# Performance work log

Hardware: AMD Instinct MI355X
Metric: run time of the kernel (lower is better)

The kernel has to match this reference:

```python
import jax, jax.numpy as jnp
import numpy as np

N_EMBD = 1024
N_HEAD = 16
HEAD_DIM = N_EMBD // N_HEAD
LN_EPS = 1e-5


def _layer_norm(x, g, b):
    mu = jnp.mean(x, axis=-1, keepdims=True)
    var = jnp.mean((x - mu) ** 2, axis=-1, keepdims=True)
    return (x - mu) * jax.lax.rsqrt(var + LN_EPS) * g + b


def setup_inputs() -> dict:
    key = jax.random.key(0)
    ks = jax.random.split(key, 12)
    C = N_EMBD
    s_in = 1.0 / np.sqrt(C)
    s_hid = 1.0 / np.sqrt(4 * C)
    return {
        "x": jax.random.normal(ks[0], (4, 2048, C), dtype=jnp.float32),
        "ln1_g": jnp.ones((C,), jnp.float32),
        "ln1_b": jnp.zeros((C,), jnp.float32),
        "ln2_g": jnp.ones((C,), jnp.float32),
        "ln2_b": jnp.zeros((C,), jnp.float32),
        "qkv_w": jax.random.uniform(ks[1], (3 * C, C), jnp.float32, -s_in, s_in),
        "qkv_b": jax.random.uniform(ks[2], (3 * C,), jnp.float32, -s_in, s_in),
        "proj_w": jax.random.uniform(ks[3], (C, C), jnp.float32, -s_in, s_in),
        "proj_b": jax.random.uniform(ks[4], (C,), jnp.float32, -s_in, s_in),
        "fc1_w": jax.random.uniform(ks[5], (4 * C, C), jnp.float32, -s_in, s_in),
        "fc1_b": jax.random.uniform(ks[6], (4 * C,), jnp.float32, -s_in, s_in),
        "fc2_w": jax.random.uniform(ks[7], (C, 4 * C), jnp.float32, -s_hid, s_hid),
        "fc2_b": jax.random.uniform(ks[8], (C,), jnp.float32, -s_hid, s_hid),
    }


def reference(x, ln1_g, ln1_b, ln2_g, ln2_b, qkv_w, qkv_b, proj_w, proj_b,
              fc1_w, fc1_b, fc2_w, fc2_b):
    B, T, C = x.shape
    # --- attention (dropout in eval mode = identity) ---
    h = _layer_norm(x, ln1_g, ln1_b)
    qkv = h @ qkv_w.T + qkv_b                      # [B,T,3C]
    qkv = qkv.reshape(B, T, 3, N_HEAD, HEAD_DIM)
    q, k, v = qkv[:, :, 0], qkv[:, :, 1], qkv[:, :, 2]   # [B,T,H,D]
    scale = 1.0 / np.sqrt(HEAD_DIM)
    attn = jnp.einsum('bqhd,bkhd->bhqk', q, k) * scale   # [B,H,T,T]
    attn = jax.nn.softmax(attn, axis=-1)
    y = jnp.einsum('bhqk,bkhd->bqhd', attn, v).reshape(B, T, C)
    x = x + (y @ proj_w.T + proj_b)
    # --- MLP ---
    h = _layer_norm(x, ln2_g, ln2_b)
    h = jax.nn.gelu(h @ fc1_w.T + fc1_b, approximate=False)
    x = x + (h @ fc2_w.T + fc2_b)
    return x
```

## Files before the change

kernel.cpp:

```cpp
#include <hip/hip_runtime.h>
#include <cstdint>
#include <cstddef>


typedef __attribute__((ext_vector_type(8))) __bf16 bf16x8;
typedef __attribute__((ext_vector_type(8))) unsigned short u16x8;
typedef __attribute__((ext_vector_type(4))) float f32x4;

static constexpr int Bn = 4;
static constexpr int Tn = 2048;
static constexpr int Cn = 1024;
static constexpr int Hn = 16;
static constexpr int Dn = 64;

__device__ __forceinline__ unsigned short f2bf(float f) {
    unsigned int u = __builtin_bit_cast(unsigned int, f);
    u += 0x7fffu + ((u >> 16) & 1u);
    return (unsigned short)(u >> 16);
}

#define GLL16(gp, lp) __builtin_amdgcn_global_load_lds( \
    (const __attribute__((address_space(1))) void*)(gp), \
    (__attribute__((address_space(3))) void*)(lp), 16, 0, 0)

__global__ __launch_bounds__(256) void conv_bf16(const float* __restrict__ in,
                                                 unsigned short* __restrict__ out,
                                                 int n4) {
    int i = blockIdx.x * 256 + threadIdx.x;
    if (i < n4) {
        float4 v = ((const float4*)in)[i];
        ushort4 o;
        o.x = f2bf(v.x); o.y = f2bf(v.y); o.z = f2bf(v.z); o.w = f2bf(v.w);
        ((ushort4*)out)[i] = o;
    }
}

__global__ __launch_bounds__(256) void ln_kernel(const float* __restrict__ x,
                                                 const float* __restrict__ g,
                                                 const float* __restrict__ b,
                                                 unsigned short* __restrict__ out) {
    __shared__ float red[8];
    const int row = blockIdx.x;
    const int tid = threadIdx.x;
    const float4 v = ((const float4*)(x + (size_t)row * Cn))[tid];
    float s = v.x + v.y + v.z + v.w;
    float q = v.x * v.x + v.y * v.y + v.z * v.z + v.w * v.w;
    #pragma unroll
    for (int m = 1; m < 64; m <<= 1) {
        s += __shfl_xor(s, m, 64);
        q += __shfl_xor(q, m, 64);
    }
    const int wave = tid >> 6;
    if ((tid & 63) == 0) { red[wave] = s; red[4 + wave] = q; }
    __syncthreads();
    s = red[0] + red[1] + red[2] + red[3];
    q = red[4] + red[5] + red[6] + red[7];
    const float mu  = s * (1.0f / Cn);
    const float var = q * (1.0f / Cn) - mu * mu;
    const float rstd = rsqrtf(var + 1e-5f);
    const float4 gv = ((const float4*)g)[tid];
    const float4 bv = ((const float4*)b)[tid];
    ushort4 o;
    o.x = f2bf((v.x - mu) * rstd * gv.x + bv.x);
    o.y = f2bf((v.y - mu) * rstd * gv.y + bv.y);
    o.z = f2bf((v.z - mu) * rstd * gv.z + bv.z);
    o.w = f2bf((v.w - mu) * rstd * gv.w + bv.w);
    ((ushort4*)(out + (size_t)row * Cn))[tid] = o;
}

template <bool GELU, bool RES>
__global__ __launch_bounds__(256, 2)
void gemm_bt(const unsigned short* __restrict__ A,
             const unsigned short* __restrict__ W,
             const float* __restrict__ bias,
             const float* __restrict__ res,
             void* __restrict__ out,
             int M, int N, int K) {
    __shared__ unsigned short aL[128 * 32];
    __shared__ unsigned short bL[128 * 32];
    const int tid  = threadIdx.x;
    const int lane = tid & 63;
    const int wave = tid >> 6;
    const int wm = wave >> 1, wn = wave & 1;
    const int bm0 = blockIdx.y * 128, bn0 = blockIdx.x * 128;
    const int l15 = lane & 15, l4 = lane >> 4;

    f32x4 acc[4][4] = {};

    for (int kt = 0; kt < K; kt += 32) {
        #pragma unroll
        for (int i = 0; i < 2; ++i) {
            const int ch = i * 256 + tid;
            const int r = ch >> 2, c = ch & 3;
            GLL16(A + (size_t)(bm0 + r) * K + kt + c * 8, &aL[ch * 8]);
            GLL16(W + (size_t)(bn0 + r) * K + kt + c * 8, &bL[ch * 8]);
        }
        __syncthreads();
        bf16x8 av[4], bv[4];
        #pragma unroll
        for (int mi = 0; mi < 4; ++mi)
            av[mi] = *(const bf16x8*)&aL[(wm * 64 + mi * 16 + l15) * 32 + l4 * 8];
        #pragma unroll
        for (int ni = 0; ni < 4; ++ni)
            bv[ni] = *(const bf16x8*)&bL[(wn * 64 + ni * 16 + l15) * 32 + l4 * 8];
        #pragma unroll
        for (int mi = 0; mi < 4; ++mi)
            #pragma unroll
            for (int ni = 0; ni < 4; ++ni)
                acc[mi][ni] = __builtin_amdgcn_mfma_f32_16x16x32_bf16(
                    av[mi], bv[ni], acc[mi][ni], 0, 0, 0);
        __syncthreads();
    }

    #pragma unroll
    for (int mi = 0; mi < 4; ++mi) {
        #pragma unroll
        for (int ni = 0; ni < 4; ++ni) {
            const int col = bn0 + wn * 64 + ni * 16 + l15;
            const float bvl = bias[col];
            #pragma unroll
            for (int j = 0; j < 4; ++j) {
                const int r = bm0 + wm * 64 + mi * 16 + l4 * 4 + j;
                float v = acc[mi][ni][j] + bvl;
                if (GELU) v = 0.5f * v * (1.0f + erff(v * 0.70710678118f));
                const size_t idx = (size_t)r * N + col;
                if (RES) ((float*)out)[idx] = res[idx] + v;
                else     ((unsigned short*)out)[idx] = f2bf(v);
            }
        }
    }
}

__global__ __launch_bounds__(256, 2)
void attn_kernel(const unsigned short* __restrict__ qkv,
                 unsigned short* __restrict__ y) {
    __shared__ unsigned short kL[128 * 64];
    __shared__ unsigned short vT[64 * 128];
    __shared__ unsigned short pL[4][16 * 128];
    const int tid  = threadIdx.x;
    const int lane = tid & 63;
    const int wave = tid >> 6;
    const int l15 = lane & 15, l4 = lane >> 4;
    const int bh = blockIdx.y, b = bh >> 4, h = bh & 15;
    const int q0 = blockIdx.x * 64;
    const size_t base = (size_t)b * Tn * (3 * Cn);

    const int tq = q0 + wave * 16 + l15;
    const unsigned short* qp = qkv + base + (size_t)tq * (3 * Cn) + h * Dn;
    const bf16x8 qf0 = *(const bf16x8*)(qp + l4 * 8);
    const bf16x8 qf1 = *(const bf16x8*)(qp + 32 + l4 * 8);

    float mr[4], lr[4];
    f32x4 o[4] = {};
    #pragma unroll
    for (int j = 0; j < 4; ++j) { mr[j] = -1e30f; lr[j] = 0.0f; }

    for (int kt = 0; kt < Tn; kt += 128) {
        #pragma unroll
        for (int i = 0; i < 4; ++i) {
            const int ch = i * 256 + tid;
            const int key = ch >> 3, cs = ch & 7;
            const int c_log = cs ^ (key & 7);
            GLL16(qkv + base + (size_t)(kt + key) * (3 * Cn) + Cn + h * Dn + c_log * 8,
                  &kL[ch * 8]);
        }
        #pragma unroll
        for (int i = 0; i < 4; ++i) {
            const int ch = i * 256 + tid;
            const int key = ch & 127, c = ch >> 7;
            const u16x8 vv = *(const u16x8*)(qkv + base + (size_t)(kt + key) * (3 * Cn)
                                             + 2 * Cn + h * Dn + c * 8);
            #pragma unroll
            for (int j = 0; j < 8; ++j) {
                const int d = c * 8 + j;
                const int ps = ((key >> 3) ^ (d & 15)) * 8 + (key & 7);
                vT[d * 128 + ps] = vv[j];
            }
        }
        __syncthreads();

        f32x4 s[8];
        __builtin_amdgcn_s_setprio(1);
        #pragma unroll
        for (int ni = 0; ni < 8; ++ni) {
            const int krow = ni * 16 + l15;
            const int ks = (krow & 7) << 3;
            const bf16x8 kb0 = *(const bf16x8*)&kL[krow * 64 + ((l4 * 8) ^ ks)];
            const bf16x8 kb1 = *(const bf16x8*)&kL[krow * 64 + ((32 + l4 * 8) ^ ks)];
            f32x4 a = {};
            a = __builtin_amdgcn_mfma_f32_16x16x32_bf16(qf0, kb0, a, 0, 0, 0);
            a = __builtin_amdgcn_mfma_f32_16x16x32_bf16(qf1, kb1, a, 0, 0, 0);
            s[ni] = a * 0.125f;
        }
        __builtin_amdgcn_s_setprio(0);

        #pragma unroll
        for (int j = 0; j < 4; ++j) {
            float tm = -1e30f;
            #pragma unroll
            for (int ni = 0; ni < 8; ++ni) tm = fmaxf(tm, s[ni][j]);
            #pragma unroll
            for (int m = 1; m < 16; m <<= 1) tm = fmaxf(tm, __shfl_xor(tm, m, 64));
            const float mn = fmaxf(mr[j], tm);
            const float al = __expf(mr[j] - mn);
            mr[j] = mn;
            float rs = 0.0f;
            #pragma unroll
            for (int ni = 0; ni < 8; ++ni) {
                const float p = __expf(s[ni][j] - mn);
                s[ni][j] = p;
                rs += p;
            }
            #pragma unroll
            for (int m = 1; m < 16; m <<= 1) rs += __shfl_xor(rs, m, 64);
            lr[j] = lr[j] * al + rs;
            #pragma unroll
            for (int di = 0; di < 4; ++di) o[di][j] *= al;
            const int row = l4 * 4 + j;
            #pragma unroll
            for (int ni = 0; ni < 8; ++ni) {
                const int col = ni * 16 + l15;
                const int ps = (((col >> 3) ^ row) << 3) | (col & 7);
                pL[wave][row * 128 + ps] = f2bf(s[ni][j]);
            }
        }

        __builtin_amdgcn_s_setprio(1);
        #pragma unroll
        for (int kk = 0; kk < 4; ++kk) {
            const int pslot = (kk * 4 + l4) ^ l15;
            const bf16x8 pa = *(const bf16x8*)&pL[wave][l15 * 128 + pslot * 8];
            #pragma unroll
            for (int di = 0; di < 4; ++di) {
                const int drow = di * 16 + l15;
                const int vslot = (kk * 4 + l4) ^ (drow & 15);
                const bf16x8 vb = *(const bf16x8*)&vT[drow * 128 + vslot * 8];
                o[di] = __builtin_amdgcn_mfma_f32_16x16x32_bf16(pa, vb, o[di], 0, 0, 0);
            }
        }
        __builtin_amdgcn_s_setprio(0);
        __syncthreads();
    }

    #pragma unroll
    for (int di = 0; di < 4; ++di) {
        #pragma unroll
        for (int j = 0; j < 4; ++j) {
            const int t = q0 + wave * 16 + l4 * 4 + j;
            y[(size_t)(b * Tn + t) * Cn + h * Dn + di * 16 + l15] = f2bf(o[di][j] / lr[j]);
        }
    }
}

extern "C" void kernel_launch(void* const* d_in, const int* in_sizes, int n_in,
                              void* d_out, int out_size, void* d_ws, size_t ws_size,
                              hipStream_t stream) {
    (void)in_sizes; (void)n_in; (void)out_size; (void)ws_size;
    const float* x      = (const float*)d_in[0];
    const float* ln1_g  = (const float*)d_in[1];
    const float* ln1_b  = (const float*)d_in[2];
    const float* ln2_g  = (const float*)d_in[3];
    const float* ln2_b  = (const float*)d_in[4];
    const float* qkv_w  = (const float*)d_in[5];
    const float* qkv_b  = (const float*)d_in[6];
    const float* proj_w = (const float*)d_in[7];
    const float* proj_b = (const float*)d_in[8];
    const float* fc1_w  = (const float*)d_in[9];
    const float* fc1_b  = (const float*)d_in[10];
    const float* fc2_w  = (const float*)d_in[11];
    const float* fc2_b  = (const float*)d_in[12];

    char* ws = (char*)d_ws;
    unsigned short* wq  = (unsigned short*)(ws + 0);
    unsigned short* wp  = (unsigned short*)(ws + 6291456);
    unsigned short* wf1 = (unsigned short*)(ws + 8388608);
    unsigned short* wf2 = (unsigned short*)(ws + 16777216);
    unsigned short* h   = (unsigned short*)(ws + 25165824);
    unsigned short* qkv = (unsigned short*)(ws + 41943040);
    unsigned short* yb  = (unsigned short*)(ws + 92274688);
    unsigned short* act = (unsigned short*)(ws + 41943040);
    float*          x2  = (float*)d_out;

    const int BT = Bn * Tn;

    conv_bf16<<<dim3(3072), dim3(256), 0, stream>>>(qkv_w, wq, 3 * Cn * Cn / 4);
    conv_bf16<<<dim3(1024), dim3(256), 0, stream>>>(proj_w, wp, Cn * Cn / 4);
    conv_bf16<<<dim3(4096), dim3(256), 0, stream>>>(fc1_w, wf1, 4 * Cn * Cn / 4);
    conv_bf16<<<dim3(4096), dim3(256), 0, stream>>>(fc2_w, wf2, 4 * Cn * Cn / 4);

    ln_kernel<<<dim3(BT), dim3(256), 0, stream>>>(x, ln1_g, ln1_b, h);
    gemm_bt<false, false><<<dim3(3 * Cn / 128, BT / 128), dim3(256), 0, stream>>>(
        h, wq, qkv_b, nullptr, qkv, BT, 3 * Cn, Cn);
    attn_kernel<<<dim3(Tn / 64, Bn * Hn), dim3(256), 0, stream>>>(qkv, yb);
    gemm_bt<false, true><<<dim3(Cn / 128, BT / 128), dim3(256), 0, stream>>>(
        yb, wp, proj_b, x, x2, BT, Cn, Cn);
    ln_kernel<<<dim3(BT), dim3(256), 0, stream>>>(x2, ln2_g, ln2_b, h);
    gemm_bt<true, false><<<dim3(4 * Cn / 128, BT / 128), dim3(256), 0, stream>>>(
        h, wf1, fc1_b, nullptr, act, BT, 4 * Cn, Cn);
    gemm_bt<false, true><<<dim3(Cn / 128, BT / 128), dim3(256), 0, stream>>>(
        act, wf2, fc2_b, x2, (float*)d_out, BT, Cn, 4 * Cn);
}
```

Before: 671.9 us.

## Rewrite GEMM as 256x256 double-buffered tiles with swizzled LDS and interleaved prefetch

Replaces the 128x128 K=32 GEMM with a 512-thread kernel that computes 256x256 tiles at K=64 per step. It double-buffers LDS with a XOR swizzle to avoid bank conflicts and spreads the next tile's global-to-LDS loads between MFMA groups under raised wave priority. The aim is more data reuse per load, fewer barriers, and hiding load latency behind compute. In exchange it uses 128KB of LDS and a large accumulator set, which may limit occupancy, and the grids for the N=1024 GEMMs become small (128 blocks).

```diff
diff --git a/kernel.cpp b/kernel.cpp
--- a/kernel.cpp
+++ b/kernel.cpp
@@ -69,58 +69,122 @@
 }
 
 template <bool GELU, bool RES>
-__global__ __launch_bounds__(256, 2)
-void gemm_bt(const unsigned short* __restrict__ A,
+__global__ __launch_bounds__(512, 2)
+void gemm256(const unsigned short* __restrict__ A,
              const unsigned short* __restrict__ W,
              const float* __restrict__ bias,
              const float* __restrict__ res,
              void* __restrict__ out,
              int M, int N, int K) {
-    __shared__ unsigned short aL[128 * 32];
-    __shared__ unsigned short bL[128 * 32];
+    __shared__ unsigned short aL[2][256 * 64];
+    __shared__ unsigned short bL[2][256 * 64];
     const int tid  = threadIdx.x;
     const int lane = tid & 63;
     const int wave = tid >> 6;
-    const int wm = wave >> 1, wn = wave & 1;
-    const int bm0 = blockIdx.y * 128, bn0 = blockIdx.x * 128;
+    const int wm = wave >> 2;
+    const int wn = wave & 3;
+    const int bm0 = blockIdx.y * 256, bn0 = blockIdx.x * 256;
     const int l15 = lane & 15, l4 = lane >> 4;
-
-    f32x4 acc[4][4] = {};
-
-    for (int kt = 0; kt < K; kt += 32) {
+    const int NT = K >> 6;
+
+    const unsigned short* srcA[2][2];
+    const unsigned short* srcB[2][2];
+    int dstc[2][2];
+    #pragma unroll
+    for (int gh = 0; gh < 2; ++gh) {
         #pragma unroll
         for (int i = 0; i < 2; ++i) {
-            const int ch = i * 256 + tid;
-            const int r = ch >> 2, c = ch & 3;
-            GLL16(A + (size_t)(bm0 + r) * K + kt + c * 8, &aL[ch * 8]);
-            GLL16(W + (size_t)(bn0 + r) * K + kt + c * 8, &bL[ch * 8]);
-        }
-        __syncthreads();
-        bf16x8 av[4], bv[4];
-        #pragma unroll
-        for (int mi = 0; mi < 4; ++mi)
-            av[mi] = *(const bf16x8*)&aL[(wm * 64 + mi * 16 + l15) * 32 + l4 * 8];
+            const int ch = i * 512 + tid;
+            const int row = ch >> 3, sl = ch & 7;
+            const int srow = gh * 128 + row;
+            const int scol = (sl ^ (srow & 7)) << 3;
+            srcA[gh][i] = A + (size_t)(bm0 + srow) * K + scol;
+            srcB[gh][i] = W + (size_t)(bn0 + srow) * K + scol;
+            dstc[gh][i] = gh * 1024 + ch;
+        }
+    }
+
+    f32x4 acc[8][4] = {};
+
+    #pragma unroll
+    for (int gh = 0; gh < 2; ++gh)
+        #pragma unroll
+        for (int i = 0; i < 2; ++i) {
+            GLL16(srcA[gh][i], &aL[0][dstc[gh][i] * 8]);
+            GLL16(srcB[gh][i], &bL[0][dstc[gh][i] * 8]);
+        }
+    asm volatile("s_waitcnt vmcnt(0)" ::: "memory");
+    __builtin_amdgcn_sched_barrier(0);
+    __builtin_amdgcn_s_barrier();
+
+    for (int t = 0; t < NT; ++t) {
+        const int cur = t & 1, nxt = cur ^ 1;
+        const bool pf = (t + 1 < NT);
+        const int kt1 = (t + 1) << 6;
+
+        if (pf) {
+            GLL16(srcA[0][0] + kt1, &aL[nxt][dstc[0][0] * 8]);
+            GLL16(srcA[0][1] + kt1, &aL[nxt][dstc[0][1] * 8]);
+        }
+        bf16x8 bfr[4][2];
         #pragma unroll
         for (int ni = 0; ni < 4; ++ni)
-            bv[ni] = *(const bf16x8*)&bL[(wn * 64 + ni * 16 + l15) * 32 + l4 * 8];
-        #pragma unroll
-        for (int mi = 0; mi < 4; ++mi)
-            #pragma unroll
-            for (int ni = 0; ni < 4; ++ni)
-                acc[mi][ni] = __builtin_amdgcn_mfma_f32_16x16x32_bf16(
-                    av[mi], bv[ni], acc[mi][ni], 0, 0, 0);
-        __syncthreads();
-    }
-
-    #pragma unroll
-    for (int mi = 0; mi < 4; ++mi) {
+            #pragma unroll
+            for (int kk = 0; kk < 2; ++kk) {
+                const int row = wn * 64 + ni * 16 + l15;
+                const int sl = (kk * 4 + l4) ^ (row & 7);
+                bfr[ni][kk] = *(const bf16x8*)&bL[cur][row * 64 + sl * 8];
+            }
+
+        #pragma unroll
+        for (int q = 0; q < 4; ++q) {
+            if (q == 1 && pf) {
+                GLL16(srcA[1][0] + kt1, &aL[nxt][dstc[1][0] * 8]);
+                GLL16(srcA[1][1] + kt1, &aL[nxt][dstc[1][1] * 8]);
+            }
+            if (q == 2 && pf) {
+                GLL16(srcB[0][0] + kt1, &bL[nxt][dstc[0][0] * 8]);
+                GLL16(srcB[0][1] + kt1, &bL[nxt][dstc[0][1] * 8]);
+            }
+            if (q == 3 && pf) {
+                GLL16(srcB[1][0] + kt1, &bL[nxt][dstc[1][0] * 8]);
+                GLL16(srcB[1][1] + kt1, &bL[nxt][dstc[1][1] * 8]);
+            }
+            bf16x8 afr[2][2];
+            #pragma unroll
+            for (int m2 = 0; m2 < 2; ++m2)
+                #pragma unroll
+                for (int kk = 0; kk < 2; ++kk) {
+                    const int row = wm * 128 + (q * 2 + m2) * 16 + l15;
+                    const int sl = (kk * 4 + l4) ^ (row & 7);
+                    afr[m2][kk] = *(const bf16x8*)&aL[cur][row * 64 + sl * 8];
+                }
+            __builtin_amdgcn_s_setprio(1);
+            #pragma unroll
+            for (int m2 = 0; m2 < 2; ++m2)
+                #pragma unroll
+                for (int ni = 0; ni < 4; ++ni)
+                    #pragma unroll
+                    for (int kk = 0; kk < 2; ++kk)
+                        acc[q * 2 + m2][ni] = __builtin_amdgcn_mfma_f32_16x16x32_bf16(
+                            afr[m2][kk], bfr[ni][kk], acc[q * 2 + m2][ni], 0, 0, 0);
+            __builtin_amdgcn_s_setprio(0);
+        }
+
+        asm volatile("s_waitcnt vmcnt(0)" ::: "memory");
+        __builtin_amdgcn_sched_barrier(0);
+        __builtin_amdgcn_s_barrier();
+    }
+
+    #pragma unroll
+    for (int mi = 0; mi < 8; ++mi) {
         #pragma unroll
         for (int ni = 0; ni < 4; ++ni) {
             const int col = bn0 + wn * 64 + ni * 16 + l15;
             const float bvl = bias[col];
             #pragma unroll
             for (int j = 0; j < 4; ++j) {
-                const int r = bm0 + wm * 64 + mi * 16 + l4 * 4 + j;
+                const int r = bm0 + wm * 128 + mi * 16 + l4 * 4 + j;
                 float v = acc[mi][ni][j] + bvl;
                 if (GELU) v = 0.5f * v * (1.0f + erff(v * 0.70710678118f));
                 const size_t idx = (size_t)r * N + col;
@@ -289,14 +353,14 @@
     conv_bf16<<<dim3(4096), dim3(256), 0, stream>>>(fc2_w, wf2, 4 * Cn * Cn / 4);
 
     ln_kernel<<<dim3(BT), dim3(256), 0, stream>>>(x, ln1_g, ln1_b, h);
-    gemm_bt<false, false><<<dim3(3 * Cn / 128, BT / 128), dim3(256), 0, stream>>>(
+    gemm256<false, false><<<dim3(3 * Cn / 256, BT / 256), dim3(512), 0, stream>>>(
         h, wq, qkv_b, nullptr, qkv, BT, 3 * Cn, Cn);
     attn_kernel<<<dim3(Tn / 64, Bn * Hn), dim3(256), 0, stream>>>(qkv, yb);
-    gemm_bt<false, true><<<dim3(Cn / 128, BT / 128), dim3(256), 0, stream>>>(
+    gemm256<false, true><<<dim3(Cn / 256, BT / 256), dim3(512), 0, stream>>>(
         yb, wp, proj_b, x, x2, BT, Cn, Cn);
     ln_kernel<<<dim3(BT), dim3(256), 0, stream>>>(x2, ln2_g, ln2_b, h);
-    gemm_bt<true, false><<<dim3(4 * Cn / 128, BT / 128), dim3(256), 0, stream>>>(
+    gemm256<true, false><<<dim3(4 * Cn / 256, BT / 256), dim3(512), 0, stream>>>(
         h, wf1, fc1_b, nullptr, act, BT, 4 * Cn, Cn);
-    gemm_bt<false, true><<<dim3(Cn / 128, BT / 128), dim3(256), 0, stream>>>(
+    gemm256<false, true><<<dim3(Cn / 256, BT / 256), dim3(512), 0, stream>>>(
         act, wf2, fc2_b, x2, (float*)d_out, BT, Cn, 4 * Cn);
 }
```

Measured after the change: 784.6 us. 1.17x slower.

## Double-buffer GEMM LDS tiles with K=64 steps and XOR-swizzled layout

Applied to the files above, without the earlier changes.

The GEMM kernel now uses two LDS buffers and issues the global-to-LDS loads for the next K tile before computing on the current one, so memory latency overlaps the MFMA work. The K step grows from 32 to 64, halving the number of barriers per tile. LDS chunks are XOR-swizzled by row to avoid bank conflicts on the fragment reads. LDS use rises to 64KB per block, which may limit the occupancy implied by launch_bounds(256,2). With a single barrier per iteration, the prefetch into the next buffer is not waited on before that buffer is read, so correctness relies on implicit ordering of the async loads.

```diff
diff --git a/kernel.cpp b/kernel.cpp
--- a/kernel.cpp
+++ b/kernel.cpp
@@ -76,39 +76,73 @@
              const float* __restrict__ res,
              void* __restrict__ out,
              int M, int N, int K) {
-    __shared__ unsigned short aL[128 * 32];
-    __shared__ unsigned short bL[128 * 32];
+    __shared__ unsigned short aL[2][128 * 64];
+    __shared__ unsigned short bL[2][128 * 64];
     const int tid  = threadIdx.x;
     const int lane = tid & 63;
     const int wave = tid >> 6;
     const int wm = wave >> 1, wn = wave & 1;
     const int bm0 = blockIdx.y * 128, bn0 = blockIdx.x * 128;
     const int l15 = lane & 15, l4 = lane >> 4;
+    const int NT = K >> 6;
+
+    const unsigned short* srcA[4];
+    const unsigned short* srcB[4];
+    #pragma unroll
+    for (int i = 0; i < 4; ++i) {
+        const int ch = i * 256 + tid;
+        const int row = ch >> 3, sl = ch & 7;
+        const int scol = (sl ^ (row & 7)) << 3;
+        srcA[i] = A + (size_t)(bm0 + row) * K + scol;
+        srcB[i] = W + (size_t)(bn0 + row) * K + scol;
+    }
 
     f32x4 acc[4][4] = {};
 
-    for (int kt = 0; kt < K; kt += 32) {
-        #pragma unroll
-        for (int i = 0; i < 2; ++i) {
-            const int ch = i * 256 + tid;
-            const int r = ch >> 2, c = ch & 3;
-            GLL16(A + (size_t)(bm0 + r) * K + kt + c * 8, &aL[ch * 8]);
-            GLL16(W + (size_t)(bn0 + r) * K + kt + c * 8, &bL[ch * 8]);
-        }
-        __syncthreads();
-        bf16x8 av[4], bv[4];
+    #pragma unroll
+    for (int i = 0; i < 4; ++i) {
+        const int ch = i * 256 + tid;
+        GLL16(srcA[i], &aL[0][ch * 8]);
+        GLL16(srcB[i], &bL[0][ch * 8]);
+    }
+    __syncthreads();
+
+    for (int t = 0; t < NT; ++t) {
+        const int cur = t & 1, nxt = cur ^ 1;
+        if (t + 1 < NT) {
+            const int kt1 = (t + 1) << 6;
+            #pragma unroll
+            for (int i = 0; i < 4; ++i) {
+                const int ch = i * 256 + tid;
+                GLL16(srcA[i] + kt1, &aL[nxt][ch * 8]);
+                GLL16(srcB[i] + kt1, &bL[nxt][ch * 8]);
+            }
+        }
+        bf16x8 av[4][2], bv[4][2];
+        #pragma unroll
+        for (int ni = 0; ni < 4; ++ni)
+            #pragma unroll
+            for (int kk = 0; kk < 2; ++kk) {
+                const int row = wn * 64 + ni * 16 + l15;
+                const int sl = (kk * 4 + l4) ^ (row & 7);
+                bv[ni][kk] = *(const bf16x8*)&bL[cur][row * 64 + sl * 8];
+            }
         #pragma unroll
         for (int mi = 0; mi < 4; ++mi)
-            av[mi] = *(const bf16x8*)&aL[(wm * 64 + mi * 16 + l15) * 32 + l4 * 8];
-        #pragma unroll
-        for (int ni = 0; ni < 4; ++ni)
-            bv[ni] = *(const bf16x8*)&bL[(wn * 64 + ni * 16 + l15) * 32 + l4 * 8];
+            #pragma unroll
+            for (int kk = 0; kk < 2; ++kk) {
+                const int row = wm * 64 + mi * 16 + l15;
+                const int sl = (kk * 4 + l4) ^ (row & 7);
+                av[mi][kk] = *(const bf16x8*)&aL[cur][row * 64 + sl * 8];
+            }
         #pragma unroll
         for (int mi = 0; mi < 4; ++mi)
             #pragma unroll
             for (int ni = 0; ni < 4; ++ni)
-                acc[mi][ni] = __builtin_amdgcn_mfma_f32_16x16x32_bf16(
-                    av[mi], bv[ni], acc[mi][ni], 0, 0, 0);
+                #pragma unroll
+                for (int kk = 0; kk < 2; ++kk)
+                    acc[mi][ni] = __builtin_amdgcn_mfma_f32_16x16x32_bf16(
+                        av[mi][kk], bv[ni][kk], acc[mi][ni], 0, 0, 0);
         __syncthreads();
     }
 
```

Measured after the change: 653.7 us. 1.03x faster.
